# Kernel optimization log

Measured on AMD Instinct MI355X. Metric: run time of the kernel, lower is better.

The kernel has to match this reference:

```python
import jax, jax.numpy as jnp
import numpy as np
import math

NUM_HEADS = 16
SEGMENT_SIZE = 128
DILATION = 2


def hilbert_map(seq_len: int) -> np.ndarray:
    """Boustrophedon ('Hilbert') permutation, matching the torch reference."""
    if seq_len <= 64:
        return np.arange(seq_len, dtype=np.int64)
    g = int(math.ceil(math.sqrt(seq_len)))
    fm = np.zeros(seq_len, dtype=np.int64)
    idx = 0
    for row in range(g):
        cols = range(g) if row % 2 == 0 else range(g - 1, -1, -1)
        for col in cols:
            lp = row * g + col
            if lp < seq_len and idx < seq_len:
                fm[lp] = idx
                idx += 1
    return fm


def setup_inputs() -> dict:
    key = jax.random.key(0)
    k1, k2, k3 = jax.random.split(key, 3)
    B, S, D = 2, 8192, 1024
    x = jax.random.normal(k1, (B, S, D), dtype=jnp.float32)
    W_qkv = jax.random.normal(k2, (D, 3 * D), dtype=jnp.float32) * 0.02
    W_out = jax.random.normal(k3, (D, D), dtype=jnp.float32) * 0.02
    return {"x": x, "W_qkv": W_qkv, "W_out": W_out}


def reference(x, W_qkv, W_out):
    B, S, Dm = x.shape
    H, Dh = NUM_HEADS, Dm // NUM_HEADS
    seg, dil = SEGMENT_SIZE, DILATION
    scale = Dh ** -0.5

    qkv = (x @ W_qkv).reshape(B, S, 3, H, Dh)
    q = jnp.transpose(qkv[:, :, 0], (0, 2, 1, 3))  # [B,H,S,Dh]
    k = jnp.transpose(qkv[:, :, 1], (0, 2, 1, 3))
    v = jnp.transpose(qkv[:, :, 2], (0, 2, 1, 3))

    # Hilbert reorder (active since S > 64)
    m = jnp.asarray(hilbert_map(S))
    q, k, v = q[:, :, m], k[:, :, m], v[:, :, m]

    # Vectorized segment-local dilated attention (S % seg == 0 here)
    nseg = S // seg
    qs = q.reshape(B, H, nseg, seg, Dh)
    ks = k.reshape(B, H, nseg, seg, Dh)[:, :, :, ::dil]  # dilated keys
    vs = v.reshape(B, H, nseg, seg, Dh)[:, :, :, ::dil]
    scores = jnp.einsum('bhnqd,bhnkd->bhnqk', qs, ks) * scale
    attn = jax.nn.softmax(scores, axis=-1)
    out = jnp.einsum('bhnqk,bhnkd->bhnqd', attn, vs).reshape(B, H, S, Dh)

    # Reverse Hilbert ordering
    inv = jnp.argsort(m)
    out = out[:, :, inv]

    out = jnp.transpose(out, (0, 2, 1, 3)).reshape(B, S, Dm)
    return out @ W_out
```

## Files before the change

kernel.cpp:

```cpp
#include <hip/hip_runtime.h>
#include <stdint.h>

typedef unsigned short ushort_t;
typedef __bf16 bf16x8 __attribute__((ext_vector_type(8)));
typedef float  f32x4  __attribute__((ext_vector_type(4)));

#define DEV static __device__ __forceinline__

DEV ushort_t f2bf(float f){
  union { float f; unsigned u; } x; x.f = f;
  unsigned u = x.u;
  return (ushort_t)((u + 0x7fffu + ((u >> 16) & 1u)) >> 16);
}

DEV int hmap(int p){
  int r = p / 91;
  int c = p - r * 91;
  return (r & 1) ? (r * 91 + 90 - c) : p;
}

DEV int arow_rt(int r, int gather){
  if (gather == 0) return r;
  if (gather == 1){ int b = r >> 13, p = r & 8191; return b * 8192 + hmap(p); }
  int b = r >> 12, rem = r & 4095, seg = rem >> 6, j = rem & 63;
  return b * 8192 + hmap(seg * 128 + 2 * j);
}

DEV void async16(const void* g, void* l){
  __builtin_amdgcn_global_load_lds(
      (const __attribute__((address_space(1))) unsigned*)g,
      (__attribute__((address_space(3))) unsigned*)l, 16, 0, 0);
}

__global__ __launch_bounds__(256) void prep_kernel(const float* __restrict__ x,
                                                   const float* __restrict__ Wqkv,
                                                   const float* __restrict__ Wout,
                                                   ushort_t* __restrict__ xb,
                                                   ushort_t* __restrict__ WqT,
                                                   ushort_t* __restrict__ WoT){
  __shared__ ushort_t t[64 * 66];
  int id = blockIdx.x, tid = threadIdx.x;
  if (id < 2048){
    const int n4 = (16384 * 1024) / 4;
    int stride = 2048 * 256;
    for (int i = id * 256 + tid; i < n4; i += stride){
      float4 v = ((const float4*)x)[i];
      ushort4 o;
      o.x = f2bf(v.x); o.y = f2bf(v.y); o.z = f2bf(v.z); o.w = f2bf(v.w);
      ((ushort4*)xb)[i] = o;
    }
    return;
  }
  const float* W; ushort_t* WT; int rows, cols, bx, by;
  if (id < 2816){ int q = id - 2048; W = Wqkv; WT = WqT; rows = 1024; cols = 3072; bx = q % 48; by = q / 48; }
  else          { int q = id - 2816; W = Wout; WT = WoT; rows = 1024; cols = 1024; bx = q % 16; by = q / 16; }
  int c0 = bx * 64, r0 = by * 64;
  int cl = tid & 63, rb = tid >> 6;
  for (int i = 0; i < 16; ++i){
    int r = rb + i * 4;
    t[r * 66 + cl] = f2bf(W[(size_t)(r0 + r) * cols + c0 + cl]);
  }
  __syncthreads();
  int rr = tid & 63, cb = tid >> 6;
  for (int i = 0; i < 16; ++i){
    int cc = cb + i * 4;
    WT[(size_t)(c0 + cc) * rows + r0 + rr] = t[rr * 66 + cc];
  }
}


#define BARRIER() asm volatile("s_barrier" ::: "memory")
#define VMCNT8()  asm volatile("s_waitcnt vmcnt(8)" ::: "memory")
#define VMCNT0()  asm volatile("s_waitcnt vmcnt(0)" ::: "memory")

#define STAGE_A_TO(DST, T1)                                                    \
  {                                                                            \
    _Pragma("unroll") for (int i = 0; i < 4; ++i)                              \
      async16(&A[asrcR[i] + (size_t)(T1) * 64], &DST[i * 4096 + tid * 8]);     \
  }

#define STAGE_B_TO(DST, T1)                                                    \
  {                                                                            \
    _Pragma("unroll") for (int i = 0; i < 4; ++i)                              \
      async16(&BT[bsrcR[i] + (size_t)(T1) * 64], &DST[i * 4096 + tid * 8]);    \
  }

#define COMPUTE(ABUF, BBUF)                                                    \
  {                                                                            \
    bf16x8 bv[4][2];                                                           \
    _Pragma("unroll") for (int ni = 0; ni < 4; ++ni)                           \
      _Pragma("unroll") for (int kk = 0; kk < 2; ++kk)                         \
        bv[ni][kk] = *(const bf16x8*)&BBUF[(wn * 64 + ni * 16 + md) * 64 + axor[kk]]; \
    _Pragma("unroll") for (int kk = 0; kk < 2; ++kk)                           \
      _Pragma("unroll") for (int mi = 0; mi < 8; ++mi){                        \
        bf16x8 af = *(const bf16x8*)&ABUF[(wm * 128 + mi * 16 + md) * 64 + axor[kk]]; \
        _Pragma("unroll") for (int ni = 0; ni < 4; ++ni)                       \
          acc[mi][ni] = __builtin_amdgcn_mfma_f32_16x16x32_bf16(               \
              af, bv[ni][kk], acc[mi][ni], 0, 0, 0);                           \
      }                                                                        \
  }

#define TILE_STEP(CUR, NXT, TSTAGE)                                            \
  {                                                                            \
    if ((TSTAGE) < NT){                                                        \
      STAGE_A_TO(As##NXT, TSTAGE); STAGE_B_TO(Bs##NXT, TSTAGE);                \
      VMCNT8();                                                                \
    } else { VMCNT0(); }                                                       \
    BARRIER();                                                                 \
    COMPUTE(As##CUR, Bs##CUR);                                                 \
    BARRIER();                                                                 \
  }

template<int OUT_BF16>
DEV void gemm_body(const ushort_t* __restrict__ A, const ushort_t* __restrict__ BT,
                   void* __restrict__ Cout, int N, int K, int gather, int m0, int n0,
                   ushort_t* As0, ushort_t* As1, ushort_t* Bs0, ushort_t* Bs1){
  const int NT = K >> 6;
  int tid = threadIdx.x;
  int lane = tid & 63, w = tid >> 6;
  int md = lane & 15, qd = lane >> 4;
  int wm = w >> 2, wn = w & 3;

  int rbase = tid >> 3;
  int g0 = ((tid & 7) ^ (rbase & 7)) * 8;
  size_t asrcR[4], bsrcR[4];
  #pragma unroll
  for (int i = 0; i < 4; ++i){
    asrcR[i] = (size_t)arow_rt(m0 + i * 64 + rbase, gather) * K + g0;
    bsrcR[i] = (size_t)(n0 + i * 64 + rbase) * K + g0;
  }

  int axor[2] = { (qd ^ (md & 7)) * 8, ((4 + qd) ^ (md & 7)) * 8 };

  f32x4 acc[8][4];
  #pragma unroll
  for (int a = 0; a < 8; ++a)
    #pragma unroll
    for (int b = 0; b < 4; ++b)
      #pragma unroll
      for (int e = 0; e < 4; ++e) acc[a][b][e] = 0.f;

  STAGE_A_TO(As0, 0);
  STAGE_B_TO(Bs0, 0);
  VMCNT0(); BARRIER();

  for (int t = 0; t < NT; t += 2){
    TILE_STEP(0, 1, t + 1);
    TILE_STEP(1, 0, t + 2);
  }

  if (OUT_BF16){
    float* wbuf = (float*)((w < 4) ? (void*)As0 : (void*)As1) + (w & 3) * 1088;
    int r16 = lane >> 4, c16 = lane & 15;
    #pragma unroll
    for (int mi = 0; mi < 8; ++mi){
      #pragma unroll
      for (int ni = 0; ni < 4; ++ni)
        #pragma unroll
        for (int reg = 0; reg < 4; ++reg)
          wbuf[(qd * 4 + reg) * 68 + ni * 16 + md] = acc[mi][ni][reg];
      #pragma unroll
      for (int rr = 0; rr < 4; ++rr){
        int row = rr * 4 + r16;
        float4 v = *(const float4*)&wbuf[row * 68 + c16 * 4];
        int grow = m0 + wm * 128 + mi * 16 + row;
        int gcol = n0 + wn * 64 + c16 * 4;
        ushort4 ob;
        ob.x = f2bf(v.x); ob.y = f2bf(v.y); ob.z = f2bf(v.z); ob.w = f2bf(v.w);
        *(ushort4*)&((ushort_t*)Cout)[(size_t)grow * N + gcol] = ob;
      }
    }
  } else {
    #pragma unroll
    for (int mi = 0; mi < 8; ++mi)
      #pragma unroll
      for (int ni = 0; ni < 4; ++ni){
        f32x4 v = acc[mi][ni];
        #pragma unroll
        for (int reg = 0; reg < 4; ++reg){
          int grow = m0 + wm * 128 + mi * 16 + qd * 4 + reg;
          int gcol = n0 + wn * 64 + ni * 16 + md;
          ((float*)Cout)[(size_t)grow * N + gcol] = v[reg];
        }
      }
  }
}

__global__ __launch_bounds__(512, 2) void gemm_qkv(const ushort_t* __restrict__ xb,
                                                   const ushort_t* __restrict__ WqT,
                                                   ushort_t* __restrict__ Qbuf,
                                                   ushort_t* __restrict__ KVbuf){
  __shared__ __align__(16) ushort_t As0[16384];
  __shared__ __align__(16) ushort_t As1[16384];
  __shared__ __align__(16) ushort_t Bs0[16384];
  __shared__ __align__(16) ushort_t Bs1[16384];
  int id = blockIdx.x;
  const ushort_t* BT; ushort_t* C; int N, gather, m0, n0;
  if (id < 256){
    int o = id;
    m0 = (o & 63) << 8; n0 = (o >> 6) << 8;
    BT = WqT; C = Qbuf; N = 1024; gather = 1;
  } else {
    int o = id - 256;
    m0 = (o & 31) << 8; n0 = (o >> 5) << 8;
    BT = WqT + (size_t)1024 * 1024; C = KVbuf; N = 2048; gather = 2;
  }
  gemm_body<1>(xb, BT, C, N, 1024, gather, m0, n0, As0, As1, Bs0, Bs1);
}

__global__ __launch_bounds__(512, 2) void gemm_out(const ushort_t* __restrict__ aoutb,
                                                   const ushort_t* __restrict__ WoT,
                                                   float* __restrict__ out){
  __shared__ __align__(16) ushort_t As0[16384];
  __shared__ __align__(16) ushort_t As1[16384];
  __shared__ __align__(16) ushort_t Bs0[16384];
  __shared__ __align__(16) ushort_t Bs1[16384];
  int o = blockIdx.x;
  int m0 = (o & 63) << 8, n0 = (o >> 6) << 8;
  gemm_body<0>(aoutb, WoT, out, 1024, 1024, 0, m0, n0, As0, As1, Bs0, Bs1);
}

__global__ __launch_bounds__(256) void attn_kernel(const ushort_t* __restrict__ Qb,
                                                   const ushort_t* __restrict__ KV,
                                                   ushort_t* __restrict__ aout){
  __shared__ ushort_t Qs[128 * 72];
  __shared__ ushort_t Ks[64 * 72];
  __shared__ ushort_t Vt[64 * 72];
  int tid  = threadIdx.x;
  int lane = tid & 63, w = tid >> 6;
  int qd = lane >> 4, md = lane & 15;
  int seg = blockIdx.x, h = blockIdx.y, b = blockIdx.z;
  int p0 = seg * 128;

  for (int it = 0; it < 4; ++it){
    int q = it * 256 + tid;
    int r = q >> 3, ch = q & 7;
    uint4 d = *(const uint4*)&Qb[(size_t)(b * 8192 + p0 + r) * 1024 + h * 64 + ch * 8];
    *(uint4*)&Qs[r * 72 + ch * 8] = d;
  }
  for (int it = 0; it < 2; ++it){
    int q = it * 256 + tid;
    int r = q >> 3, ch = q & 7;
    uint4 d = *(const uint4*)&KV[(size_t)(b * 4096 + seg * 64 + r) * 2048 + h * 64 + ch * 8];
    *(uint4*)&Ks[r * 72 + ch * 8] = d;
  }
  for (int it = 0; it < 2; ++it){
    int q = it * 256 + tid;
    int r = q >> 3, ch = q & 7;
    union { uint4 v; ushort_t u[8]; } d;
    d.v = *(const uint4*)&KV[(size_t)(b * 4096 + seg * 64 + r) * 2048 + 1024 + h * 64 + ch * 8];
    int kslot = ((r >> 3) ^ ch) * 8 + (r & 7);
    for (int e = 0; e < 8; ++e) Vt[(ch * 8 + e) * 72 + kslot] = d.u[e];
  }
  __syncthreads();

  f32x4 z = {0.f, 0.f, 0.f, 0.f};
  f32x4 sc[2][4];
  for (int mi = 0; mi < 2; ++mi) for (int ni = 0; ni < 4; ++ni) sc[mi][ni] = z;
  for (int kc = 0; kc < 2; ++kc){
    bf16x8 aq[2], bk[4];
    for (int mi = 0; mi < 2; ++mi)
      aq[mi] = *(const bf16x8*)&Qs[(w * 32 + mi * 16 + md) * 72 + kc * 32 + qd * 8];
    for (int ni = 0; ni < 4; ++ni)
      bk[ni] = *(const bf16x8*)&Ks[(ni * 16 + md) * 72 + kc * 32 + qd * 8];
    for (int mi = 0; mi < 2; ++mi)
      for (int ni = 0; ni < 4; ++ni)
        sc[mi][ni] = __builtin_amdgcn_mfma_f32_16x16x32_bf16(aq[mi], bk[ni], sc[mi][ni], 0, 0, 0);
  }

  const float scale = 0.125f;
  ushort_t* Ps = Qs;
  for (int mi = 0; mi < 2; ++mi){
    for (int i = 0; i < 4; ++i){
      float mx = sc[mi][0][i];
      for (int ni = 1; ni < 4; ++ni) mx = fmaxf(mx, sc[mi][ni][i]);
      for (int d = 1; d < 16; d <<= 1) mx = fmaxf(mx, __shfl_xor(mx, d));
      float e[4], sum = 0.f;
      for (int ni = 0; ni < 4; ++ni){ e[ni] = __expf((sc[mi][ni][i] - mx) * scale); sum += e[ni]; }
      for (int d = 1; d < 16; d <<= 1) sum += __shfl_xor(sum, d);
      float inv = 1.0f / sum;
      int r = w * 32 + mi * 16 + qd * 4 + i;
      for (int ni = 0; ni < 4; ++ni)
        Ps[r * 72 + ni * 16 + md] = f2bf(e[ni] * inv);
    }
  }

  f32x4 oc[2][4];
  for (int mi = 0; mi < 2; ++mi) for (int ni = 0; ni < 4; ++ni) oc[mi][ni] = z;
  for (int kc = 0; kc < 2; ++kc){
    bf16x8 ap[2], bv[4];
    for (int mi = 0; mi < 2; ++mi)
      ap[mi] = *(const bf16x8*)&Ps[(w * 32 + mi * 16 + md) * 72 + kc * 32 + qd * 8];
    for (int ni = 0; ni < 4; ++ni){
      int dd = ni * 16 + md;
      int vchunk = ((kc * 4 + qd) ^ ((dd >> 3) & 7)) & 7;
      bv[ni] = *(const bf16x8*)&Vt[dd * 72 + vchunk * 8];
    }
    for (int mi = 0; mi < 2; ++mi)
      for (int ni = 0; ni < 4; ++ni)
        oc[mi][ni] = __builtin_amdgcn_mfma_f32_16x16x32_bf16(ap[mi], bv[ni], oc[mi][ni], 0, 0, 0);
  }

  for (int mi = 0; mi < 2; ++mi){
    for (int i = 0; i < 4; ++i){
      int rl = w * 32 + mi * 16 + qd * 4 + i;
      for (int ni = 0; ni < 4; ++ni)
        Ps[rl * 72 + ni * 16 + md] = f2bf(oc[mi][ni][i]);
    }
  }
  __syncthreads();
  for (int it = 0; it < 4; ++it){
    int q = it * 256 + tid;
    int r = q >> 3, ch = q & 7;
    int s = hmap(p0 + r);
    *(uint4*)&aout[(size_t)(b * 8192 + s) * 1024 + h * 64 + ch * 8] =
        *(const uint4*)&Qs[r * 72 + ch * 8];
  }
}

extern "C" void kernel_launch(void* const* d_in, const int* in_sizes, int n_in,
                              void* d_out, int out_size, void* d_ws, size_t ws_size,
                              hipStream_t stream){
  const float* x    = (const float*)d_in[0];
  const float* Wqkv = (const float*)d_in[1];
  const float* Wout = (const float*)d_in[2];
  float* out = (float*)d_out;

  char* ws = (char*)d_ws;
  ushort_t* xb    = (ushort_t*)(ws);
  ushort_t* WqT   = (ushort_t*)(ws + 33554432);
  ushort_t* WoT   = (ushort_t*)(ws + 39845888);
  ushort_t* Qbuf  = (ushort_t*)(ws + 41943040);
  ushort_t* KVbuf = (ushort_t*)(ws + 75497472);
  ushort_t* aoutb = (ushort_t*)(ws + 109051904);

  prep_kernel<<<3072, 256, 0, stream>>>(x, Wqkv, Wout, xb, WqT, WoT);
  gemm_qkv<<<512, 512, 0, stream>>>(xb, WqT, Qbuf, KVbuf);
  attn_kernel<<<dim3(64, 16, 2), 256, 0, stream>>>(Qbuf, KVbuf, aoutb);
  gemm_out<<<256, 512, 0, stream>>>(aoutb, WoT, out);
}
```

Baseline: 260.0 us.

## Make attention blocks persistent over four segments with register prefetch of next tile

The attention kernel now launches 512 blocks, each processing four consecutive (segment, head, batch) jobs instead of one job per block. While one job is being computed, the Q/K/V tiles for the next job are loaded from global memory into registers, then written to shared memory after the current output is stored. This is meant to hide global load latency behind MFMA and softmax work, at the cost of more registers, extra barriers and fewer blocks in flight.

Result: slower. 274.1 us (+5.4%).

```diff
diff --git a/kernel.cpp b/kernel.cpp
--- a/kernel.cpp
+++ b/kernel.cpp
@@ -67,7 +67,6 @@
     WT[(size_t)(c0 + cc) * rows + r0 + rr] = t[rr * 66 + cc];
   }
 }
-
 
 #define BARRIER() asm volatile("s_barrier" ::: "memory")
 #define VMCNT8()  asm volatile("s_waitcnt vmcnt(8)" ::: "memory")
@@ -220,6 +219,38 @@
   gemm_body<0>(aoutb, WoT, out, 1024, 1024, 0, m0, n0, As0, As1, Bs0, Bs1);
 }
 
+#define LOADJOB(J)                                                             \
+  {                                                                            \
+    int seg_ = (J) & 63, h_ = ((J) >> 6) & 15, b_ = (J) >> 10;                 \
+    int p0_ = seg_ * 128;                                                      \
+    _Pragma("unroll") for (int i2 = 0; i2 < 4; ++i2){                          \
+      int q = i2 * 256 + tid, r = q >> 3, ch = q & 7;                          \
+      qreg[i2] = *(const uint4*)&Qb[(size_t)(b_ * 8192 + p0_ + r) * 1024 + h_ * 64 + ch * 8]; \
+    }                                                                          \
+    _Pragma("unroll") for (int i2 = 0; i2 < 2; ++i2){                          \
+      int q = i2 * 256 + tid, r = q >> 3, ch = q & 7;                          \
+      size_t rowb_ = (size_t)(b_ * 4096 + seg_ * 64 + r) * 2048 + h_ * 64;     \
+      kreg[i2] = *(const uint4*)&KV[rowb_ + ch * 8];                           \
+      vreg[i2] = *(const uint4*)&KV[rowb_ + 1024 + ch * 8];                    \
+    }                                                                          \
+  }
+
+#define WRITEJOB()                                                             \
+  {                                                                            \
+    _Pragma("unroll") for (int i2 = 0; i2 < 4; ++i2){                          \
+      int q = i2 * 256 + tid, r = q >> 3, ch = q & 7;                          \
+      *(uint4*)&Qs[r * 72 + ch * 8] = qreg[i2];                                \
+    }                                                                          \
+    _Pragma("unroll") for (int i2 = 0; i2 < 2; ++i2){                          \
+      int q = i2 * 256 + tid, r = q >> 3, ch = q & 7;                          \
+      *(uint4*)&Ks[r * 72 + ch * 8] = kreg[i2];                                \
+      union { uint4 v; ushort_t u[8]; } d; d.v = vreg[i2];                     \
+      int kslot = ((r >> 3) ^ ch) * 8 + (r & 7);                               \
+      _Pragma("unroll") for (int e = 0; e < 8; ++e)                            \
+        Vt[(ch * 8 + e) * 72 + kslot] = d.u[e];                                \
+    }                                                                          \
+  }
+
 __global__ __launch_bounds__(256) void attn_kernel(const ushort_t* __restrict__ Qb,
                                                    const ushort_t* __restrict__ KV,
                                                    ushort_t* __restrict__ aout){
@@ -229,92 +260,89 @@
   int tid  = threadIdx.x;
   int lane = tid & 63, w = tid >> 6;
   int qd = lane >> 4, md = lane & 15;
-  int seg = blockIdx.x, h = blockIdx.y, b = blockIdx.z;
-  int p0 = seg * 128;
+
+  uint4 qreg[4], kreg[2], vreg[2];
+  int j0 = blockIdx.x * 4;
+
+  LOADJOB(j0);
+  WRITEJOB();
+  __syncthreads();
 
   for (int it = 0; it < 4; ++it){
-    int q = it * 256 + tid;
-    int r = q >> 3, ch = q & 7;
-    uint4 d = *(const uint4*)&Qb[(size_t)(b * 8192 + p0 + r) * 1024 + h * 64 + ch * 8];
-    *(uint4*)&Qs[r * 72 + ch * 8] = d;
-  }
-  for (int it = 0; it < 2; ++it){
-    int q = it * 256 + tid;
-    int r = q >> 3, ch = q & 7;
-    uint4 d = *(const uint4*)&KV[(size_t)(b * 4096 + seg * 64 + r) * 2048 + h * 64 + ch * 8];
-    *(uint4*)&Ks[r * 72 + ch * 8] = d;
-  }
-  for (int it = 0; it < 2; ++it){
-    int q = it * 256 + tid;
-    int r = q >> 3, ch = q & 7;
-    union { uint4 v; ushort_t u[8]; } d;
-    d.v = *(const uint4*)&KV[(size_t)(b * 4096 + seg * 64 + r) * 2048 + 1024 + h * 64 + ch * 8];
-    int kslot = ((r >> 3) ^ ch) * 8 + (r & 7);
-    for (int e = 0; e < 8; ++e) Vt[(ch * 8 + e) * 72 + kslot] = d.u[e];
-  }
-  __syncthreads();
-
-  f32x4 z = {0.f, 0.f, 0.f, 0.f};
-  f32x4 sc[2][4];
-  for (int mi = 0; mi < 2; ++mi) for (int ni = 0; ni < 4; ++ni) sc[mi][ni] = z;
-  for (int kc = 0; kc < 2; ++kc){
-    bf16x8 aq[2], bk[4];
-    for (int mi = 0; mi < 2; ++mi)
-      aq[mi] = *(const bf16x8*)&Qs[(w * 32 + mi * 16 + md) * 72 + kc * 32 + qd * 8];
-    for (int ni = 0; ni < 4; ++ni)
-      bk[ni] = *(const bf16x8*)&Ks[(ni * 16 + md) * 72 + kc * 32 + qd * 8];
-    for (int mi = 0; mi < 2; ++mi)
+    int j = j0 + it;
+    int seg = j & 63, h = (j >> 6) & 15, b = j >> 10;
+    int p0 = seg * 128;
+
+    if (it < 3) LOADJOB(j0 + it + 1);
+
+    f32x4 z = {0.f, 0.f, 0.f, 0.f};
+    f32x4 sc[2][4];
+    for (int mi = 0; mi < 2; ++mi) for (int ni = 0; ni < 4; ++ni) sc[mi][ni] = z;
+    for (int kc = 0; kc < 2; ++kc){
+      bf16x8 aq[2], bk[4];
+      for (int mi = 0; mi < 2; ++mi)
+        aq[mi] = *(const bf16x8*)&Qs[(w * 32 + mi * 16 + md) * 72 + kc * 32 + qd * 8];
       for (int ni = 0; ni < 4; ++ni)
-        sc[mi][ni] = __builtin_amdgcn_mfma_f32_16x16x32_bf16(aq[mi], bk[ni], sc[mi][ni], 0, 0, 0);
-  }
-
-  const float scale = 0.125f;
-  ushort_t* Ps = Qs;
-  for (int mi = 0; mi < 2; ++mi){
-    for (int i = 0; i < 4; ++i){
-      float mx = sc[mi][0][i];
-      for (int ni = 1; ni < 4; ++ni) mx = fmaxf(mx, sc[mi][ni][i]);
-      for (int d = 1; d < 16; d <<= 1) mx = fmaxf(mx, __shfl_xor(mx, d));
-      float e[4], sum = 0.f;
-      for (int ni = 0; ni < 4; ++ni){ e[ni] = __expf((sc[mi][ni][i] - mx) * scale); sum += e[ni]; }
-      for (int d = 1; d < 16; d <<= 1) sum += __shfl_xor(sum, d);
-      float inv = 1.0f / sum;
-      int r = w * 32 + mi * 16 + qd * 4 + i;
-      for (int ni = 0; ni < 4; ++ni)
-        Ps[r * 72 + ni * 16 + md] = f2bf(e[ni] * inv);
-    }
-  }
-
-  f32x4 oc[2][4];
-  for (int mi = 0; mi < 2; ++mi) for (int ni = 0; ni < 4; ++ni) oc[mi][ni] = z;
-  for (int kc = 0; kc < 2; ++kc){
-    bf16x8 ap[2], bv[4];
-    for (int mi = 0; mi < 2; ++mi)
-      ap[mi] = *(const bf16x8*)&Ps[(w * 32 + mi * 16 + md) * 72 + kc * 32 + qd * 8];
-    for (int ni = 0; ni < 4; ++ni){
-      int dd = ni * 16 + md;
-      int vchunk = ((kc * 4 + qd) ^ ((dd >> 3) & 7)) & 7;
-      bv[ni] = *(const bf16x8*)&Vt[dd * 72 + vchunk * 8];
-    }
-    for (int mi = 0; mi < 2; ++mi)
-      for (int ni = 0; ni < 4; ++ni)
-        oc[mi][ni] = __builtin_amdgcn_mfma_f32_16x16x32_bf16(ap[mi], bv[ni], oc[mi][ni], 0, 0, 0);
-  }
-
-  for (int mi = 0; mi < 2; ++mi){
-    for (int i = 0; i < 4; ++i){
-      int rl = w * 32 + mi * 16 + qd * 4 + i;
-      for (int ni = 0; ni < 4; ++ni)
-        Ps[rl * 72 + ni * 16 + md] = f2bf(oc[mi][ni][i]);
-    }
-  }
-  __syncthreads();
-  for (int it = 0; it < 4; ++it){
-    int q = it * 256 + tid;
-    int r = q >> 3, ch = q & 7;
-    int s = hmap(p0 + r);
-    *(uint4*)&aout[(size_t)(b * 8192 + s) * 1024 + h * 64 + ch * 8] =
-        *(const uint4*)&Qs[r * 72 + ch * 8];
+        bk[ni] = *(const bf16x8*)&Ks[(ni * 16 + md) * 72 + kc * 32 + qd * 8];
+      for (int mi = 0; mi < 2; ++mi)
+        for (int ni = 0; ni < 4; ++ni)
+          sc[mi][ni] = __builtin_amdgcn_mfma_f32_16x16x32_bf16(aq[mi], bk[ni], sc[mi][ni], 0, 0, 0);
+    }
+
+    const float scale = 0.125f;
+    ushort_t* Ps = Qs;
+    for (int mi = 0; mi < 2; ++mi){
+      for (int i = 0; i < 4; ++i){
+        float mx = sc[mi][0][i];
+        for (int ni = 1; ni < 4; ++ni) mx = fmaxf(mx, sc[mi][ni][i]);
+        for (int d = 1; d < 16; d <<= 1) mx = fmaxf(mx, __shfl_xor(mx, d));
+        float e[4], sum = 0.f;
+        for (int ni = 0; ni < 4; ++ni){ e[ni] = __expf((sc[mi][ni][i] - mx) * scale); sum += e[ni]; }
+        for (int d = 1; d < 16; d <<= 1) sum += __shfl_xor(sum, d);
+        float inv = 1.0f / sum;
+        int r = w * 32 + mi * 16 + qd * 4 + i;
+        for (int ni = 0; ni < 4; ++ni)
+          Ps[r * 72 + ni * 16 + md] = f2bf(e[ni] * inv);
+      }
+    }
+
+    f32x4 oc[2][4];
+    for (int mi = 0; mi < 2; ++mi) for (int ni = 0; ni < 4; ++ni) oc[mi][ni] = z;
+    for (int kc = 0; kc < 2; ++kc){
+      bf16x8 ap[2], bv[4];
+      for (int mi = 0; mi < 2; ++mi)
+        ap[mi] = *(const bf16x8*)&Ps[(w * 32 + mi * 16 + md) * 72 + kc * 32 + qd * 8];
+      for (int ni = 0; ni < 4; ++ni){
+        int dd = ni * 16 + md;
+        int vchunk = ((kc * 4 + qd) ^ ((dd >> 3) & 7)) & 7;
+        bv[ni] = *(const bf16x8*)&Vt[dd * 72 + vchunk * 8];
+      }
+      for (int mi = 0; mi < 2; ++mi)
+        for (int ni = 0; ni < 4; ++ni)
+          oc[mi][ni] = __builtin_amdgcn_mfma_f32_16x16x32_bf16(ap[mi], bv[ni], oc[mi][ni], 0, 0, 0);
+    }
+
+    for (int mi = 0; mi < 2; ++mi){
+      for (int i = 0; i < 4; ++i){
+        int rl = w * 32 + mi * 16 + qd * 4 + i;
+        for (int ni = 0; ni < 4; ++ni)
+          Ps[rl * 72 + ni * 16 + md] = f2bf(oc[mi][ni][i]);
+      }
+    }
+    __syncthreads();
+    for (int it2 = 0; it2 < 4; ++it2){
+      int q = it2 * 256 + tid;
+      int r = q >> 3, ch = q & 7;
+      int s = hmap(p0 + r);
+      *(uint4*)&aout[(size_t)(b * 8192 + s) * 1024 + h * 64 + ch * 8] =
+          *(const uint4*)&Qs[r * 72 + ch * 8];
+    }
+
+    if (it < 3){
+      __syncthreads();
+      WRITEJOB();
+      __syncthreads();
+    }
   }
 }
 
@@ -336,6 +364,6 @@
 
   prep_kernel<<<3072, 256, 0, stream>>>(x, Wqkv, Wout, xb, WqT, WoT);
   gemm_qkv<<<512, 512, 0, stream>>>(xb, WqT, Qbuf, KVbuf);
-  attn_kernel<<<dim3(64, 16, 2), 256, 0, stream>>>(Qbuf, KVbuf, aoutb);
+  attn_kernel<<<512, 256, 0, stream>>>(Qbuf, KVbuf, aoutb);
   gemm_out<<<256, 512, 0, stream>>>(aoutb, WoT, out);
 }
```
